# Optimization experiments

Measured on AMD Instinct MI355X. Metric: run time of the kernel, lower is better.

## Reference

```python
import jax, jax.numpy as jnp
import numpy as np

N = 50000      # nodes
E = 800000     # edges (avg degree 16)
IN_DIM = 128
H = 4          # attention heads
D = 32         # hidden dim per head
NEG_SLOPE = 0.2


def setup_inputs() -> dict:
    key = jax.random.key(0)
    ks = jax.random.split(key, 9)
    x = jax.random.normal(ks[0], (N, IN_DIM), dtype=jnp.float32)
    src = jax.random.randint(ks[1], (E,), 0, N, dtype=jnp.int64)
    dst = jax.random.randint(ks[2], (E,), 0, N, dtype=jnp.int64)
    # layer 0: IN_DIM -> H*D ; layer 1: H*D -> H*D
    s0 = 1.0 / np.sqrt(IN_DIM)
    s1 = 1.0 / np.sqrt(H * D)
    W1 = jax.random.normal(ks[3], (H * D, IN_DIM), dtype=jnp.float32) * s0
    al1 = jax.random.normal(ks[4], (1, H, D), dtype=jnp.float32) * s1
    ar1 = jax.random.normal(ks[5], (1, H, D), dtype=jnp.float32) * s1
    W2 = jax.random.normal(ks[6], (H * D, H * D), dtype=jnp.float32) * s1
    al2 = jax.random.normal(ks[7], (1, H, D), dtype=jnp.float32) * s1
    ar2 = jax.random.normal(ks[8], (1, H, D), dtype=jnp.float32) * s1
    return {"x": x, "src": src, "dst": dst, "W1": W1, "al1": al1, "ar1": ar1,
            "W2": W2, "al2": al2, "ar2": ar2}


def gat_conv(h, src, dst, W, al, ar):
    """DGL-style GATConv. h: [N, F_in] -> [N, H, D], with ELU activation."""
    feat = (h @ W.T).reshape(N, H, D)                 # [N,H,D]
    el = jnp.sum(feat * al, axis=-1)                  # [N,H] a_l . Wh
    er = jnp.sum(feat * ar, axis=-1)                  # [N,H] a_r . Wh
    e = jax.nn.leaky_relu(el[src] + er[dst], NEG_SLOPE)  # [E,H]
    # numerically stable edge softmax over incoming edges of each dst node
    m = jax.ops.segment_max(e, dst, num_segments=N)   # [N,H]
    ee = jnp.exp(e - m[dst])                          # [E,H]
    denom = jax.ops.segment_sum(ee, dst, num_segments=N)  # [N,H]
    alpha = ee / denom[dst]                           # [E,H]
    msg = feat[src] * alpha[..., None]                # [E,H,D]
    out = jax.ops.segment_sum(msg, dst, num_segments=N)   # [N,H,D]
    return jax.nn.elu(out)


def reference(x, src, dst, W1, al1, ar1, W2, al2, ar2):
    h = gat_conv(x, src, dst, W1, al1, ar1).reshape(N, H * D)  # flatten(1)
    h = gat_conv(h, src, dst, W2, al2, ar2)                    # [N,H,D]
    return jnp.mean(h, axis=1)                                 # [N,D]
```

## Files before the change

kernel.cpp:

```cpp
#include <hip/hip_runtime.h>
#include <cmath>
#include <type_traits>

#define HEADS 4
#define FDIM 128
#define NEG 0.2f
#define NBUCK 8
#define EPT 16

typedef __attribute__((ext_vector_type(8))) __bf16 bf16x8;
typedef __attribute__((ext_vector_type(8))) _Float16 h16x8;
typedef __attribute__((ext_vector_type(4))) float f32x4;

__global__ __launch_bounds__(256) void prep_kernel(
    const float* __restrict__ W1, const float* __restrict__ al1,
    const float* __restrict__ ar1,
    const float* __restrict__ W2, const float* __restrict__ al2,
    const float* __restrict__ ar2,
    __bf16* __restrict__ wf1, __bf16* __restrict__ wext1,
    _Float16* __restrict__ wf2, _Float16* __restrict__ wext2,
    int* __restrict__ counts, int nb)
{
    const int b = blockIdx.x, tid = threadIdx.x;
    if (b < 256) {
        int idx = (b & 127) * 256 + tid;
        int j = idx & 7;
        int r = idx >> 3;
        int c = r & 15; r >>= 4;
        int t = r & 7;  r >>= 3;
        int kq = r & 15;
        int hl = r >> 4;
        if (b < 128) {
            float v = W1[(t * 16 + c) * 128 + kq * 8 + j];
            __bf16 hi = (__bf16)v;
            wf1[idx] = (hl == 0) ? hi : (__bf16)(v - (float)hi);
        } else {
            float v = W2[(t * 16 + c) * 128 + kq * 8 + j];
            _Float16 hi = (_Float16)v;
            wf2[idx] = (hl == 0) ? hi : (_Float16)(v - (float)hi);
        }
    } else if (b < 258) {
        const float* W  = (b == 256) ? W1 : W2;
        const float* al = (b == 256) ? al1 : al2;
        const float* ar = (b == 256) ? ar1 : ar2;
        __shared__ float val[1024];
        #pragma unroll
        for (int ch = 0; ch < 4; ++ch) {
            int idx = ch * 256 + tid;
            int c = idx >> 7, k = idx & 127;
            int h = c & 3;
            const float* a = (c < 4) ? al : ar;
            float s = 0.f;
            for (int d = 0; d < 32; ++d)
                s += a[h * 32 + d] * W[(h * 32 + d) * 128 + k];
            val[c * 128 + k] = s;
        }
        __syncthreads();
        #pragma unroll
        for (int ch = 0; ch < 16; ++ch) {
            int idx = tid * 16 + ch;
            int j = idx & 7;
            int r = idx >> 3;
            int c = r & 15; r >>= 4;
            int kq = r & 15;
            int hl = r >> 4;
            float v = (c < 8) ? val[c * 128 + kq * 8 + j] : 0.f;
            if (b == 256) {
                __bf16 hi = (__bf16)v;
                wext1[idx] = (hl == 0) ? hi : (__bf16)(v - (float)hi);
            } else {
                _Float16 hi = (_Float16)v;
                wext2[idx] = (hl == 0) ? hi : (_Float16)(v - (float)hi);
            }
        }
    } else {
        int i0 = ((b - 258) * 256 + tid) * 4;
        if (i0 + 3 < nb) {
            *(int4*)&counts[i0] = make_int4(0, 0, 0, 0);
        } else {
            for (int i = i0; i < nb; ++i) counts[i] = 0;
        }
    }
}

__device__ __forceinline__ void gemm_body_f32(
    const float* __restrict__ X, const bf16x8* __restrict__ wf,
    const bf16x8* __restrict__ wext, _Float16* __restrict__ featH,
    float* __restrict__ el, float* __restrict__ er,
    int nnodes, int tile0, int tend, int stride, bf16x8* lw)
{
    const int tid = threadIdx.x;
    const int wave = tid >> 6, lane = tid & 63;
    const int l15 = lane & 15, quad = lane >> 4;

    int tile = tile0;
    float xr[32], xn[32];

    auto loadX = [&](int tl, float* dst) {
        int nodeA = tl * 64 + wave * 16 + l15;
        bool v = nodeA < nnodes;
        const float4* xp = (const float4*)(X + (size_t)nodeA * 128);
        #pragma unroll
        for (int ks = 0; ks < 4; ++ks) {
            float4 a = v ? xp[ks * 8 + quad * 2]     : make_float4(0.f, 0.f, 0.f, 0.f);
            float4 b = v ? xp[ks * 8 + quad * 2 + 1] : make_float4(0.f, 0.f, 0.f, 0.f);
            dst[ks * 8 + 0] = a.x; dst[ks * 8 + 1] = a.y;
            dst[ks * 8 + 2] = a.z; dst[ks * 8 + 3] = a.w;
            dst[ks * 8 + 4] = b.x; dst[ks * 8 + 5] = b.y;
            dst[ks * 8 + 6] = b.z; dst[ks * 8 + 7] = b.w;
        }
    };

    loadX(tile, xr);
    for (int i = tid; i < 2048; i += 256) lw[i] = wf[i];
    __syncthreads();

    while (true) {
        int next = tile + stride;
        if (next < tend) loadX(next, xn);

        f32x4 acc[9];
        #pragma unroll
        for (int t = 0; t < 9; ++t) acc[t] = (f32x4){0.f, 0.f, 0.f, 0.f};

        #pragma unroll
        for (int ks = 0; ks < 4; ++ks) {
            bf16x8 ahi, alo;
            #pragma unroll
            for (int j = 0; j < 8; ++j) {
                float xv = xr[ks * 8 + j];
                __bf16 h = (__bf16)xv;
                ahi[j] = h;
                alo[j] = (__bf16)(xv - (float)h);
            }
            const int kq = ks * 4 + quad;

            {
                bf16x8 bh = wext[(kq) * 16 + l15];
                bf16x8 bl = wext[(16 + kq) * 16 + l15];
                acc[8] = __builtin_amdgcn_mfma_f32_16x16x32_bf16(ahi, bh, acc[8], 0, 0, 0);
                acc[8] = __builtin_amdgcn_mfma_f32_16x16x32_bf16(alo, bh, acc[8], 0, 0, 0);
                acc[8] = __builtin_amdgcn_mfma_f32_16x16x32_bf16(ahi, bl, acc[8], 0, 0, 0);
            }
            #pragma unroll
            for (int t = 0; t < 8; ++t) {
                bf16x8 bh = lw[(kq * 8 + t) * 16 + l15];
                bf16x8 bl = wf[2048 + (kq * 8 + t) * 16 + l15];
                acc[t] = __builtin_amdgcn_mfma_f32_16x16x32_bf16(ahi, bh, acc[t], 0, 0, 0);
                acc[t] = __builtin_amdgcn_mfma_f32_16x16x32_bf16(alo, bh, acc[t], 0, 0, 0);
                acc[t] = __builtin_amdgcn_mfma_f32_16x16x32_bf16(ahi, bl, acc[t], 0, 0, 0);
            }
        }

        const int nodeC = tile * 64 + wave * 16 + quad * 4;
        #pragma unroll
        for (int r = 0; r < 4; ++r) {
            int gn = nodeC + r;
            if (gn < nnodes) {
                #pragma unroll
                for (int t = 0; t < 8; ++t)
                    featH[(size_t)gn * 128 + t * 16 + l15] = (_Float16)acc[t][r];
            }
        }
        if (l15 < 8) {
            #pragma unroll
            for (int r = 0; r < 4; ++r) {
                int gn = nodeC + r;
                if (gn < nnodes) {
                    if (l15 < 4) el[gn * HEADS + l15] = acc[8][r];
                    else         er[gn * HEADS + (l15 - 4)] = acc[8][r];
                }
            }
        }

        if (next >= tend) break;
        #pragma unroll
        for (int i = 0; i < 32; ++i) xr[i] = xn[i];
        tile = next;
    }
}

__device__ __forceinline__ void gemm_body_f16(
    const _Float16* __restrict__ X, const h16x8* __restrict__ wf,
    const h16x8* __restrict__ wext, _Float16* __restrict__ featH,
    float* __restrict__ el, float* __restrict__ er,
    int nnodes, int tile0, int tend, int stride, h16x8* lw)
{
    const int tid = threadIdx.x;
    const int wave = tid >> 6, lane = tid & 63;
    const int l15 = lane & 15, quad = lane >> 4;

    int tile = tile0;
    h16x8 xr[4], xn[4];

    auto loadX = [&](int tl, h16x8* dst) {
        int nodeA = tl * 64 + wave * 16 + l15;
        bool v = nodeA < nnodes;
        const h16x8* xp = (const h16x8*)(X + (size_t)nodeA * 128);
        #pragma unroll
        for (int ks = 0; ks < 4; ++ks) {
            if (v) {
                dst[ks] = xp[ks * 4 + quad];
            } else {
                #pragma unroll
                for (int j = 0; j < 8; ++j) dst[ks][j] = (_Float16)0.f;
            }
        }
    };

    loadX(tile, xr);
    for (int i = tid; i < 2048; i += 256) lw[i] = wf[i];
    __syncthreads();

    while (true) {
        int next = tile + stride;
        if (next < tend) loadX(next, xn);

        f32x4 acc[9];
        #pragma unroll
        for (int t = 0; t < 9; ++t) acc[t] = (f32x4){0.f, 0.f, 0.f, 0.f};

        #pragma unroll
        for (int ks = 0; ks < 4; ++ks) {
            h16x8 a = xr[ks];
            const int kq = ks * 4 + quad;
            {
                h16x8 bh = wext[(kq) * 16 + l15];
                h16x8 bl = wext[(16 + kq) * 16 + l15];
                acc[8] = __builtin_amdgcn_mfma_f32_16x16x32_f16(a, bh, acc[8], 0, 0, 0);
                acc[8] = __builtin_amdgcn_mfma_f32_16x16x32_f16(a, bl, acc[8], 0, 0, 0);
            }
            #pragma unroll
            for (int t = 0; t < 8; ++t) {
                h16x8 bh = lw[(kq * 8 + t) * 16 + l15];
                h16x8 bl = wf[2048 + (kq * 8 + t) * 16 + l15];
                acc[t] = __builtin_amdgcn_mfma_f32_16x16x32_f16(a, bh, acc[t], 0, 0, 0);
                acc[t] = __builtin_amdgcn_mfma_f32_16x16x32_f16(a, bl, acc[t], 0, 0, 0);
            }
        }

        const int nodeC = tile * 64 + wave * 16 + quad * 4;
        #pragma unroll
        for (int r = 0; r < 4; ++r) {
            int gn = nodeC + r;
            if (gn < nnodes) {
                #pragma unroll
                for (int t = 0; t < 8; ++t)
                    featH[(size_t)gn * 128 + t * 16 + l15] = (_Float16)acc[t][r];
            }
        }
        if (l15 < 8) {
            #pragma unroll
            for (int r = 0; r < 4; ++r) {
                int gn = nodeC + r;
                if (gn < nnodes) {
                    if (l15 < 4) el[gn * HEADS + l15] = acc[8][r];
                    else         er[gn * HEADS + (l15 - 4)] = acc[8][r];
                }
            }
        }

        if (next >= tend) break;
        #pragma unroll
        for (int i = 0; i < 4; ++i) xr[i] = xn[i];
        tile = next;
    }
}

__device__ __forceinline__ void hist_body(
    const int* __restrict__ src, const int* __restrict__ dst,
    int* __restrict__ counts, int nedges, int shift, int b)
{
    int i0 = (b * 256 + threadIdx.x) * EPT;
    if (i0 + EPT - 1 < nedges) {
        int s[EPT], d[EPT];
        #pragma unroll
        for (int q = 0; q < EPT / 4; ++q) {
            *(int4*)&s[q * 4] = *(const int4*)&src[i0 + q * 4];
            *(int4*)&d[q * 4] = *(const int4*)&dst[i0 + q * 4];
        }
        #pragma unroll
        for (int q = 0; q < EPT; ++q)
            atomicAdd(&counts[d[q] * NBUCK + (s[q] >> shift)], 1);
    } else {
        for (int i = i0; i < nedges; ++i)
            atomicAdd(&counts[dst[i] * NBUCK + (src[i] >> shift)], 1);
    }
}

__device__ __forceinline__ void scatter_body(
    const int* __restrict__ src, const int* __restrict__ dst,
    int* __restrict__ cursor, int* __restrict__ csr_src,
    int nedges, int shift, int b)
{
    int i0 = (b * 256 + threadIdx.x) * EPT;
    if (i0 + EPT - 1 < nedges) {
        int s[EPT], d[EPT], p[EPT];
        #pragma unroll
        for (int q = 0; q < EPT / 4; ++q) {
            *(int4*)&s[q * 4] = *(const int4*)&src[i0 + q * 4];
            *(int4*)&d[q * 4] = *(const int4*)&dst[i0 + q * 4];
        }
        #pragma unroll
        for (int q = 0; q < EPT; ++q)
            p[q] = atomicAdd(&cursor[d[q] * NBUCK + (s[q] >> shift)], 1);
        #pragma unroll
        for (int q = 0; q < EPT; ++q)
            csr_src[p[q]] = s[q];
    } else {
        for (int i = i0; i < nedges; ++i)
            csr_src[atomicAdd(&cursor[dst[i] * NBUCK + (src[i] >> shift)], 1)] = src[i];
    }
}

__global__ __launch_bounds__(256) void fused_gemm_hist(
    const float* __restrict__ X, const bf16x8* __restrict__ wf,
    const bf16x8* __restrict__ wext, _Float16* __restrict__ featH,
    float* __restrict__ el, float* __restrict__ er, int nnodes,
    int t0, int tend, int gemm_blocks, int edge_blocks,
    const int* __restrict__ src, const int* __restrict__ dst,
    int* __restrict__ counts, int nedges, int shift)
{
    __shared__ bf16x8 lw[2048];
    if ((int)blockIdx.x >= edge_blocks)
        gemm_body_f32(X, wf, wext, featH, el, er, nnodes,
                      t0 + (blockIdx.x - edge_blocks), tend, gemm_blocks, lw);
    else
        hist_body(src, dst, counts, nedges, shift, blockIdx.x);
}

__global__ __launch_bounds__(256) void fused_gemm_scatter(
    const float* __restrict__ X, const bf16x8* __restrict__ wf,
    const bf16x8* __restrict__ wext, _Float16* __restrict__ featH,
    float* __restrict__ el, float* __restrict__ er, int nnodes,
    int t0, int tend, int gemm_blocks, int edge_blocks,
    const int* __restrict__ src, const int* __restrict__ dst,
    int* __restrict__ cursor, int* __restrict__ csr_src, int nedges, int shift)
{
    __shared__ bf16x8 lw[2048];
    if ((int)blockIdx.x >= edge_blocks)
        gemm_body_f32(X, wf, wext, featH, el, er, nnodes,
                      t0 + (blockIdx.x - edge_blocks), tend, gemm_blocks, lw);
    else
        scatter_body(src, dst, cursor, csr_src, nedges, shift, blockIdx.x);
}

__global__ __launch_bounds__(256) void gemm_mfma_f16_kernel(
    const _Float16* __restrict__ X, const h16x8* __restrict__ wf,
    const h16x8* __restrict__ wext, _Float16* __restrict__ featH,
    float* __restrict__ el, float* __restrict__ er, int nnodes, int ntiles)
{
    __shared__ h16x8 lw[2048];
    gemm_body_f16(X, wf, wext, featH, el, er, nnodes,
                  blockIdx.x, ntiles, gridDim.x, lw);
}

__global__ __launch_bounds__(256) void scan1_kernel(
    const int* __restrict__ counts, int* __restrict__ offsets,
    int* __restrict__ bsums, int n)
{
    __shared__ int wsums[4];
    const int tid = threadIdx.x, lane = tid & 63, w = tid >> 6;
    const int i = blockIdx.x * 1024 + tid * 4;

    int4 v = make_int4(0, 0, 0, 0);
    if (i + 3 < n) v = *(const int4*)&counts[i];
    else {
        if (i < n)     v.x = counts[i];
        if (i + 1 < n) v.y = counts[i + 1];
        if (i + 2 < n) v.z = counts[i + 2];
    }
    int s0 = v.x, s1 = s0 + v.y, s2 = s1 + v.z, s3 = s2 + v.w;

    int x = s3;
    #pragma unroll
    for (int off = 1; off < 64; off <<= 1) {
        int t = __shfl_up(x, off, 64);
        if (lane >= off) x += t;
    }
    if (lane == 63) wsums[w] = x;
    __syncthreads();
    int wbase = 0;
    #pragma unroll
    for (int k = 0; k < 4; ++k) if (k < w) wbase += wsums[k];

    int tbase = wbase + x - s3;
    if (i < n)     offsets[i]     = tbase;
    if (i + 1 < n) offsets[i + 1] = tbase + s0;
    if (i + 2 < n) offsets[i + 2] = tbase + s1;
    if (i + 3 < n) offsets[i + 3] = tbase + s2;
    if (tid == 255) bsums[blockIdx.x] = wbase + x;
}

__global__ __launch_bounds__(256) void scan23_kernel(
    int* __restrict__ offsets, int* __restrict__ cursor,
    const int* __restrict__ bsums, int n, int nedges)
{
    __shared__ int sbase;
    const int tid = threadIdx.x, b = blockIdx.x;
    if (tid < 64) {
        int s = 0;
        for (int i = tid; i < b; i += 64) s += bsums[i];
        #pragma unroll
        for (int off = 1; off < 64; off <<= 1) s += __shfl_xor(s, off, 64);
        if (tid == 0) sbase = s;
    }
    __syncthreads();
    const int base = sbase;
    const int i = b * 1024 + tid * 4;
    #pragma unroll
    for (int k = 0; k < 4; ++k)
        if (i + k < n) {
            int o = offsets[i + k] + base;
            offsets[i + k] = o;
            cursor[i + k] = o;
        }
    if (b == 0 && tid == 0) offsets[n] = nedges;
}

template <bool MEAN>
__global__ __launch_bounds__(256) void aggregate_kernel(
    const _Float16* __restrict__ featH, const float* __restrict__ el,
    const float* __restrict__ er, const int* __restrict__ offsets,
    const int* __restrict__ csr_src, void* __restrict__ outp, int nnodes)
{
    const int n = (blockIdx.x * 256 + threadIdx.x) >> 6;
    if (n >= nnodes) return;
    const int lane = threadIdx.x & 63;
    const int g = lane >> 4, u = lane & 15, h = u >> 2;
    const int beg = offsets[n * NBUCK], end = offsets[n * NBUCK + NBUCK];
    const float ern = er[n * HEADS + h];
    const int iters = (end - beg + 3) >> 2;

    float a[8];
    #pragma unroll
    for (int p = 0; p < 8; ++p) a[p] = 0.f;
    float sw = 0.f;

    const h16x8* __restrict__ frow = (const h16x8*)featH;

    int ja = beg + g;
    int jb = ja + 4;
    bool va = ja < end, vb = jb < end;
    int sa = va ? csr_src[ja] : 0;
    int sb = vb ? csr_src[jb] : 0;
    float qa = el[sa * HEADS + h];
    float qb = el[sb * HEADS + h];
    h16x8 fa = frow[(size_t)sa * 16 + u];
    h16x8 fb = frow[(size_t)sb * 16 + u];

    for (int it = 0; it < iters; ++it) {
        int jc = ja + 8;
        bool vc = jc < end;
        int sc = vc ? csr_src[jc] : 0;
        float qc = el[sc * HEADS + h];
        h16x8 fc = frow[(size_t)sc * 16 + u];

        float e = qa + ern;
        e = e > 0.f ? e : NEG * e;
        float w2 = va ? __expf(e) : 0.f;
        #pragma unroll
        for (int p = 0; p < 8; ++p) a[p] += w2 * (float)fa[p];
        sw += w2;

        ja = jb; va = vb; sa = sb; qa = qb; fa = fb;
        jb = jc; vb = vc; sb = sc; qb = qc; fb = fc;
    }

    #pragma unroll
    for (int p = 0; p < 8; ++p) {
        a[p] += __shfl_xor(a[p], 16, 64);
        a[p] += __shfl_xor(a[p], 32, 64);
    }
    sw += __shfl_xor(sw, 16, 64);
    sw += __shfl_xor(sw, 32, 64);

    float inv = sw > 0.f ? 1.f / sw : 0.f;
    float r[8];
    #pragma unroll
    for (int p = 0; p < 8; ++p) {
        float t = a[p] * inv;
        r[p] = t > 0.f ? t : __expf(t) - 1.f;
    }

    if (!MEAN) {
        if (g == 0) {
            h16x8 o;
            #pragma unroll
            for (int p = 0; p < 8; ++p) o[p] = (_Float16)r[p];
            ((h16x8*)outp)[(size_t)n * 16 + u] = o;
        }
    } else {
        #pragma unroll
        for (int p = 0; p < 8; ++p) {
            r[p] += __shfl_xor(r[p], 4, 64);
            r[p] += __shfl_xor(r[p], 8, 64);
        }
        if (g == 0 && u < 4) {
            float* out = (float*)outp;
            float4* o4 = (float4*)(out + (size_t)n * 32 + u * 8);
            o4[0] = make_float4(0.25f * r[0], 0.25f * r[1], 0.25f * r[2], 0.25f * r[3]);
            o4[1] = make_float4(0.25f * r[4], 0.25f * r[5], 0.25f * r[6], 0.25f * r[7]);
        }
    }
}

extern "C" void kernel_launch(void* const* d_in, const int* in_sizes, int n_in,
                              void* d_out, int out_size, void* d_ws, size_t ws_size,
                              hipStream_t stream)
{
    const float* x   = (const float*)d_in[0];
    const int*   src = (const int*)d_in[1];
    const int*   dst = (const int*)d_in[2];
    const float* W1  = (const float*)d_in[3];
    const float* al1 = (const float*)d_in[4];
    const float* ar1 = (const float*)d_in[5];
    const float* W2  = (const float*)d_in[6];
    const float* al2 = (const float*)d_in[7];
    const float* ar2 = (const float*)d_in[8];

    const int N = in_sizes[0] / FDIM;
    const int E = in_sizes[1];
    const int NB = N * NBUCK;

    int shift = 0;
    while (((N - 1) >> shift) > (NBUCK - 1)) ++shift;

    _Float16* h1 = (_Float16*)d_ws;
    _Float16* featH = h1 + (size_t)N * FDIM;
    float* el = (float*)(featH + (size_t)N * FDIM);
    float* er = el + (size_t)N * HEADS;
    int* counts  = (int*)(er + (size_t)N * HEADS);
    int* offsets = counts + NB;
    int* cursor  = offsets + (NB + 1);
    int* csr_src = cursor + NB;
    int* bsums   = csr_src + E;
    uintptr_t wp = ((uintptr_t)(bsums + 512) + 63) & ~(uintptr_t)63;
    __bf16* wf1     = (__bf16*)wp;
    __bf16* wext1   = wf1 + 32768;
    _Float16* wf2   = (_Float16*)(wext1 + 4096);
    _Float16* wext2 = wf2 + 32768;

    const int ntiles = (N + 63) / 64;
    const int halfT  = (ntiles + 1) / 2;
    const int gA = halfT < 256 ? halfT : 256;
    const int gB = (ntiles - halfT) < 256 ? (ntiles - halfT) : 256;
    const int edge_grid = ((E + EPT - 1) / EPT + 255) / 256;
    const int agg_grid  = (N + 3) / 4;
    const int nscan     = (NB + 1023) / 1024;
    const int zblocks   = ((NB + 3) / 4 + 255) / 256;
    const int g2 = ntiles < 512 ? ntiles : 512;

    prep_kernel<<<258 + zblocks, 256, 0, stream>>>(
        W1, al1, ar1, W2, al2, ar2, wf1, wext1, wf2, wext2, counts, NB);

    fused_gemm_hist<<<edge_grid + gA, 256, 0, stream>>>(
        x, (const bf16x8*)wf1, (const bf16x8*)wext1, featH, el, er, N,
        0, halfT, gA, edge_grid, src, dst, counts, E, shift);

    scan1_kernel<<<nscan, 256, 0, stream>>>(counts, offsets, bsums, NB);
    scan23_kernel<<<nscan, 256, 0, stream>>>(offsets, cursor, bsums, NB, E);

    fused_gemm_scatter<<<edge_grid + gB, 256, 0, stream>>>(
        x, (const bf16x8*)wf1, (const bf16x8*)wext1, featH, el, er, N,
        halfT, ntiles, gB, edge_grid, src, dst, cursor, csr_src, E, shift);

    aggregate_kernel<false><<<agg_grid, 256, 0, stream>>>(
        featH, el, er, offsets, csr_src, (void*)h1, N);

    gemm_mfma_f16_kernel<<<g2, 256, 0, stream>>>(
        h1, (const h16x8*)wf2, (const h16x8*)wext2, featH, el, er, N, ntiles);
    aggregate_kernel<true><<<agg_grid, 256, 0, stream>>>(
        featH, el, er, offsets, csr_src, d_out, N);
}
```

Baseline: 260.2 us.

## Partition edge histogram and scatter by XCC with per-XCC queues and workgroup-scope atomics

```diff
diff --git a/kernel.cpp b/kernel.cpp
--- a/kernel.cpp
+++ b/kernel.cpp
@@ -6,7 +6,9 @@
 #define FDIM 128
 #define NEG 0.2f
 #define NBUCK 8
+#define NSEG 64
 #define EPT 16
+#define XCC_GETREG 63508
 
 typedef __attribute__((ext_vector_type(8))) __bf16 bf16x8;
 typedef __attribute__((ext_vector_type(8))) _Float16 h16x8;
@@ -19,7 +21,7 @@
     const float* __restrict__ ar2,
     __bf16* __restrict__ wf1, __bf16* __restrict__ wext1,
     _Float16* __restrict__ wf2, _Float16* __restrict__ wext2,
-    int* __restrict__ counts, int nb)
+    int* __restrict__ counts, int nb, int* __restrict__ aux, int naux)
 {
     const int b = blockIdx.x, tid = threadIdx.x;
     if (b < 256) {
@@ -74,6 +76,9 @@
             }
         }
     } else {
+        if (b == 258) {
+            for (int k = tid; k < naux; k += 256) aux[k] = 0;
+        }
         int i0 = ((b - 258) * 256 + tid) * 4;
         if (i0 + 3 < nb) {
             *(int4*)&counts[i0] = make_int4(0, 0, 0, 0);
@@ -269,9 +274,11 @@
 
 __device__ __forceinline__ void hist_body(
     const int* __restrict__ src, const int* __restrict__ dst,
-    int* __restrict__ counts, int nedges, int shift, int b)
+    int* __restrict__ counts, int2* __restrict__ queue, int* __restrict__ qtail,
+    int qcap, int nedges, int shift, int b, int x)
 {
     int i0 = (b * 256 + threadIdx.x) * EPT;
+    int2* qx = queue + (size_t)x * qcap;
     if (i0 + EPT - 1 < nedges) {
         int s[EPT], d[EPT];
         #pragma unroll
@@ -279,37 +286,72 @@
             *(int4*)&s[q * 4] = *(const int4*)&src[i0 + q * 4];
             *(int4*)&d[q * 4] = *(const int4*)&dst[i0 + q * 4];
         }
+        int base = __hip_atomic_fetch_add(&qtail[x], EPT, __ATOMIC_RELAXED,
+                                          __HIP_MEMORY_SCOPE_WORKGROUP);
         #pragma unroll
         for (int q = 0; q < EPT; ++q)
-            atomicAdd(&counts[d[q] * NBUCK + (s[q] >> shift)], 1);
-    } else {
-        for (int i = i0; i < nedges; ++i)
-            atomicAdd(&counts[dst[i] * NBUCK + (src[i] >> shift)], 1);
+            qx[base + q] = make_int2(s[q], d[q]);
+        #pragma unroll
+        for (int q = 0; q < EPT; ++q)
+            (void)__hip_atomic_fetch_add(
+                &counts[(d[q] << 6) + ((s[q] >> shift) << 3) + x], 1,
+                __ATOMIC_RELAXED, __HIP_MEMORY_SCOPE_WORKGROUP);
+    } else if (i0 < nedges) {
+        int cnt = nedges - i0;
+        int base = __hip_atomic_fetch_add(&qtail[x], cnt, __ATOMIC_RELAXED,
+                                          __HIP_MEMORY_SCOPE_WORKGROUP);
+        for (int k = 0; k < cnt; ++k) {
+            int s = src[i0 + k], d = dst[i0 + k];
+            qx[base + k] = make_int2(s, d);
+            (void)__hip_atomic_fetch_add(
+                &counts[(d << 6) + ((s >> shift) << 3) + x], 1,
+                __ATOMIC_RELAXED, __HIP_MEMORY_SCOPE_WORKGROUP);
+        }
     }
 }
 
 __device__ __forceinline__ void scatter_body(
-    const int* __restrict__ src, const int* __restrict__ dst,
-    int* __restrict__ cursor, int* __restrict__ csr_src,
-    int nedges, int shift, int b)
-{
-    int i0 = (b * 256 + threadIdx.x) * EPT;
-    if (i0 + EPT - 1 < nedges) {
-        int s[EPT], d[EPT], p[EPT];
-        #pragma unroll
-        for (int q = 0; q < EPT / 4; ++q) {
-            *(int4*)&s[q * 4] = *(const int4*)&src[i0 + q * 4];
-            *(int4*)&d[q * 4] = *(const int4*)&dst[i0 + q * 4];
-        }
-        #pragma unroll
-        for (int q = 0; q < EPT; ++q)
-            p[q] = atomicAdd(&cursor[d[q] * NBUCK + (s[q] >> shift)], 1);
-        #pragma unroll
-        for (int q = 0; q < EPT; ++q)
-            csr_src[p[q]] = s[q];
-    } else {
-        for (int i = i0; i < nedges; ++i)
-            csr_src[atomicAdd(&cursor[dst[i] * NBUCK + (src[i] >> shift)], 1)] = src[i];
+    const int2* __restrict__ queue, const int* __restrict__ qtail,
+    int* __restrict__ claim, int* __restrict__ cursor,
+    int* __restrict__ csr_src, int qcap, int shift, int x)
+{
+    const int lane = threadIdx.x & 63;
+    const int nq = qtail[x];
+    const int2* qx = queue + (size_t)x * qcap;
+    while (true) {
+        int c = 0;
+        if (lane == 0)
+            c = __hip_atomic_fetch_add(&claim[x], 1, __ATOMIC_RELAXED,
+                                       __HIP_MEMORY_SCOPE_WORKGROUP);
+        c = __builtin_amdgcn_readfirstlane(c);
+        const int start = c * 1024;
+        if (start >= nq) break;
+        const int i0 = start + lane * 16;
+        if (i0 + 15 < nq) {
+            const int4* qp = (const int4*)(qx + i0);
+            int4 e[8];
+            #pragma unroll
+            for (int j = 0; j < 8; ++j) e[j] = qp[j];
+            #pragma unroll
+            for (int j = 0; j < 8; ++j) {
+                int bin0 = (e[j].y << 6) + ((e[j].x >> shift) << 3) + x;
+                int bin1 = (e[j].w << 6) + ((e[j].z >> shift) << 3) + x;
+                int p0 = __hip_atomic_fetch_add(&cursor[bin0], 1, __ATOMIC_RELAXED,
+                                                __HIP_MEMORY_SCOPE_WORKGROUP);
+                int p1 = __hip_atomic_fetch_add(&cursor[bin1], 1, __ATOMIC_RELAXED,
+                                                __HIP_MEMORY_SCOPE_WORKGROUP);
+                csr_src[p0] = e[j].x;
+                csr_src[p1] = e[j].z;
+            }
+        } else {
+            for (int i = i0; i < nq && i < i0 + 16; ++i) {
+                int2 e = qx[i];
+                int bin = (e.y << 6) + ((e.x >> shift) << 3) + x;
+                int p = __hip_atomic_fetch_add(&cursor[bin], 1, __ATOMIC_RELAXED,
+                                               __HIP_MEMORY_SCOPE_WORKGROUP);
+                csr_src[p] = e.x;
+            }
+        }
     }
 }
 
@@ -319,14 +361,18 @@
     float* __restrict__ el, float* __restrict__ er, int nnodes,
     int t0, int tend, int gemm_blocks, int edge_blocks,
     const int* __restrict__ src, const int* __restrict__ dst,
-    int* __restrict__ counts, int nedges, int shift)
+    int* __restrict__ counts, int2* __restrict__ queue,
+    int* __restrict__ qtail, int qcap, int nedges, int shift)
 {
     __shared__ bf16x8 lw[2048];
     if ((int)blockIdx.x >= edge_blocks)
         gemm_body_f32(X, wf, wext, featH, el, er, nnodes,
                       t0 + (blockIdx.x - edge_blocks), tend, gemm_blocks, lw);
-    else
-        hist_body(src, dst, counts, nedges, shift, blockIdx.x);
+    else {
+        int x = (int)(__builtin_amdgcn_s_getreg(XCC_GETREG) & 7u);
+        hist_body(src, dst, counts, queue, qtail, qcap, nedges, shift,
+                  blockIdx.x, x);
+    }
 }
 
 __global__ __launch_bounds__(256) void fused_gemm_scatter(
@@ -334,15 +380,18 @@
     const bf16x8* __restrict__ wext, _Float16* __restrict__ featH,
     float* __restrict__ el, float* __restrict__ er, int nnodes,
     int t0, int tend, int gemm_blocks, int edge_blocks,
-    const int* __restrict__ src, const int* __restrict__ dst,
-    int* __restrict__ cursor, int* __restrict__ csr_src, int nedges, int shift)
+    const int2* __restrict__ queue, const int* __restrict__ qtail,
+    int* __restrict__ claim, int* __restrict__ cursor,
+    int* __restrict__ csr_src, int qcap, int shift)
 {
     __shared__ bf16x8 lw[2048];
     if ((int)blockIdx.x >= edge_blocks)
         gemm_body_f32(X, wf, wext, featH, el, er, nnodes,
                       t0 + (blockIdx.x - edge_blocks), tend, gemm_blocks, lw);
-    else
-        scatter_body(src, dst, cursor, csr_src, nedges, shift, blockIdx.x);
+    else {
+        int x = (int)(__builtin_amdgcn_s_getreg(XCC_GETREG) & 7u);
+        scatter_body(queue, qtail, claim, cursor, csr_src, qcap, shift, x);
+    }
 }
 
 __global__ __launch_bounds__(256) void gemm_mfma_f16_kernel(
@@ -428,7 +477,7 @@
     if (n >= nnodes) return;
     const int lane = threadIdx.x & 63;
     const int g = lane >> 4, u = lane & 15, h = u >> 2;
-    const int beg = offsets[n * NBUCK], end = offsets[n * NBUCK + NBUCK];
+    const int beg = offsets[n * NSEG], end = offsets[n * NSEG + NSEG];
     const float ern = er[n * HEADS + h];
     const int iters = (end - beg + 3) >> 2;
 
@@ -521,7 +570,7 @@
 
     const int N = in_sizes[0] / FDIM;
     const int E = in_sizes[1];
-    const int NB = N * NBUCK;
+    const int NB_T = N * NSEG;
 
     int shift = 0;
     while (((N - 1) >> shift) > (NBUCK - 1)) ++shift;
@@ -530,12 +579,16 @@
     _Float16* featH = h1 + (size_t)N * FDIM;
     float* el = (float*)(featH + (size_t)N * FDIM);
     float* er = el + (size_t)N * HEADS;
-    int* counts  = (int*)(er + (size_t)N * HEADS);
-    int* offsets = counts + NB;
-    int* cursor  = offsets + (NB + 1);
-    int* csr_src = cursor + NB;
+    uintptr_t qp = ((uintptr_t)(er + (size_t)N * HEADS) + 15) & ~(uintptr_t)15;
+    int2* queue  = (int2*)qp;
+    int* counts  = (int*)(queue + (size_t)8 * E);
+    int* offsets = counts + NB_T;
+    int* cursor  = offsets + (NB_T + 1);
+    int* csr_src = cursor + NB_T;
     int* bsums   = csr_src + E;
-    uintptr_t wp = ((uintptr_t)(bsums + 512) + 63) & ~(uintptr_t)63;
+    int* qtail   = bsums + 4096;
+    int* claim   = qtail + 8;
+    uintptr_t wp = ((uintptr_t)(claim + 8) + 63) & ~(uintptr_t)63;
     __bf16* wf1     = (__bf16*)wp;
     __bf16* wext1   = wf1 + 32768;
     _Float16* wf2   = (_Float16*)(wext1 + 4096);
@@ -545,25 +598,28 @@
     const int halfT  = (ntiles + 1) / 2;
     const int gA = halfT < 256 ? halfT : 256;
     const int gB = (ntiles - halfT) < 256 ? (ntiles - halfT) : 256;
-    const int edge_grid = ((E + EPT - 1) / EPT + 255) / 256;
+    const int hist_grid = ((E + EPT - 1) / EPT + 255) / 256;
+    const int scat_grid = 512;
     const int agg_grid  = (N + 3) / 4;
-    const int nscan     = (NB + 1023) / 1024;
-    const int zblocks   = ((NB + 3) / 4 + 255) / 256;
+    const int nscan     = (NB_T + 1023) / 1024;
+    const int zblocks   = ((NB_T + 3) / 4 + 255) / 256;
     const int g2 = ntiles < 512 ? ntiles : 512;
 
     prep_kernel<<<258 + zblocks, 256, 0, stream>>>(
-        W1, al1, ar1, W2, al2, ar2, wf1, wext1, wf2, wext2, counts, NB);
-
-    fused_gemm_hist<<<edge_grid + gA, 256, 0, stream>>>(
+        W1, al1, ar1, W2, al2, ar2, wf1, wext1, wf2, wext2,
+        counts, NB_T, bsums, 4096 + 16);
+
+    fused_gemm_hist<<<hist_grid + gA, 256, 0, stream>>>(
         x, (const bf16x8*)wf1, (const bf16x8*)wext1, featH, el, er, N,
-        0, halfT, gA, edge_grid, src, dst, counts, E, shift);
-
-    scan1_kernel<<<nscan, 256, 0, stream>>>(counts, offsets, bsums, NB);
-    scan23_kernel<<<nscan, 256, 0, stream>>>(offsets, cursor, bsums, NB, E);
-
-    fused_gemm_scatter<<<edge_grid + gB, 256, 0, stream>>>(
+        0, halfT, gA, hist_grid, src, dst, counts, queue, qtail, E, E, shift);
+
+    scan1_kernel<<<nscan, 256, 0, stream>>>(counts, offsets, bsums, NB_T);
+    scan23_kernel<<<nscan, 256, 0, stream>>>(offsets, cursor, bsums, NB_T, E);
+
+    fused_gemm_scatter<<<scat_grid + gB, 256, 0, stream>>>(
         x, (const bf16x8*)wf1, (const bf16x8*)wext1, featH, el, er, N,
-        halfT, ntiles, gB, edge_grid, src, dst, cursor, csr_src, E, shift);
+        halfT, ntiles, gB, scat_grid, queue, qtail, claim, cursor,
+        csr_src, E, shift);
 
     aggregate_kernel<false><<<agg_grid, 256, 0, stream>>>(
         featH, el, er, offsets, csr_src, (void*)h1, N);
```

Result: slower. 300.0 us (+15.3%).
